# Performance work log

Hardware: AMD Instinct MI355X
Metric: run time of the kernel (lower is better)

Reference implementation:

```python
import jax, jax.numpy as jnp
import numpy as np

N, E, C = 50000, 800000, 192
H1, H2, HF = 256, 512, 512  # grapher mid, grapher conv out, ffn hidden
EPS = 1e-5


def _lin_init(k, out_f, in_f, bias=True):
    s = 1.0 / np.sqrt(in_f)
    kw, kb = jax.random.split(k)
    W = jax.random.uniform(kw, (out_f, in_f), jnp.float32, -s, s)
    if bias:
        b = jax.random.uniform(kb, (out_f,), jnp.float32, -s, s)
        return W, b
    return W


def setup_inputs() -> dict:
    key = jax.random.key(0)
    ks = jax.random.split(key, 10)
    inp = {}
    inp["x"] = jax.random.normal(ks[0], (N, C), jnp.float32)
    inp["edge_index"] = jax.random.randint(ks[1], (2, E), 0, N, jnp.int32)
    # Grapher fc1: Linear(C,256)+BN(256)
    inp["w_g1"], inp["b_g1"] = _lin_init(ks[2], H1, C)
    inp["g1_gamma"], inp["g1_beta"] = jnp.ones((H1,), jnp.float32), jnp.zeros((H1,), jnp.float32)
    # GraphConv(256, 512): lin_rel (with bias) on aggregated neighbors, lin_root (no bias) on self
    inp["w_rel"], inp["b_rel"] = _lin_init(ks[3], H2, H1)
    inp["w_root"] = _lin_init(ks[4], H2, H1, bias=False)
    # Grapher fc2: Linear(512,C)+BN(C)
    inp["w_g2"], inp["b_g2"] = _lin_init(ks[5], C, H2)
    inp["g2_gamma"], inp["g2_beta"] = jnp.ones((C,), jnp.float32), jnp.zeros((C,), jnp.float32)
    # FFN fc1: Linear(C,512)+BN(512)
    inp["w_f1"], inp["b_f1"] = _lin_init(ks[6], HF, C)
    inp["f1_gamma"], inp["f1_beta"] = jnp.ones((HF,), jnp.float32), jnp.zeros((HF,), jnp.float32)
    # FFN fc2: Linear(512,C)+BN(C)
    inp["w_f2"], inp["b_f2"] = _lin_init(ks[7], C, HF)
    inp["f2_gamma"], inp["f2_beta"] = jnp.ones((C,), jnp.float32), jnp.zeros((C,), jnp.float32)
    return inp


def _bn(x, gamma, beta):
    # BatchNorm1d in training mode: biased batch stats over the node dim
    mu = jnp.mean(x, axis=0)
    var = jnp.var(x, axis=0)
    return gamma * (x - mu) * jax.lax.rsqrt(var + EPS) + beta


def reference(x, edge_index, w_g1, b_g1, g1_gamma, g1_beta, w_rel, b_rel, w_root,
              w_g2, b_g2, g2_gamma, g2_beta, w_f1, b_f1, f1_gamma, f1_beta,
              w_f2, b_f2, f2_gamma, f2_beta):
    # ---- Grapher ----
    shortcut = x
    t = _bn(x @ w_g1.T + b_g1, g1_gamma, g1_beta)            # [N, 256]
    src, dst = edge_index[0], edge_index[1]
    agg = jax.ops.segment_sum(t[src], dst, num_segments=t.shape[0])  # [N, 256] 'add' aggregation
    h = agg @ w_rel.T + b_rel + t @ w_root.T                  # [N, 512]
    h = _bn(h @ w_g2.T + b_g2, g2_gamma, g2_beta)             # [N, C]
    x = h + shortcut
    # ---- FFN ----
    shortcut = x
    f = _bn(x @ w_f1.T + b_f1, f1_gamma, f1_beta)             # [N, 512]
    f = jax.nn.gelu(f, approximate=False)
    f = _bn(f @ w_f2.T + b_f2, f2_gamma, f2_beta)             # [N, C]
    return f + shortcut
```

## Files before the change

### kernel.cpp

```cpp
#include <hip/hip_runtime.h>
#include <hip/hip_bf16.h>
#include <math.h>

#define NN 50000
#define EE 800000
#define CC 192

typedef __attribute__((ext_vector_type(4))) float f32x4;
typedef __attribute__((ext_vector_type(8))) short bfx8;
typedef __attribute__((ext_vector_type(8))) unsigned short u16x8;

static __device__ __forceinline__ unsigned short f2bf(float f) {
    return __builtin_bit_cast(unsigned short, __float2bfloat16(f));
}
static __device__ __forceinline__ float b2f(unsigned short u) {
    unsigned v = ((unsigned)u) << 16;
    return __builtin_bit_cast(float, v);
}

template <int MODE>
static __device__ __forceinline__ bfx8 stage_row(const void* Ap, size_t off, int kc,
                                                 const float* __restrict__ Av,
                                                 const float* __restrict__ Bv)
{
    if constexpr (MODE == 1) {
        const float* A = (const float*)Ap;
        float4 u0 = *(const float4*)&A[off], u1 = *(const float4*)&A[off + 4];
        return bfx8{(short)f2bf(u0.x), (short)f2bf(u0.y), (short)f2bf(u0.z), (short)f2bf(u0.w),
                    (short)f2bf(u1.x), (short)f2bf(u1.y), (short)f2bf(u1.z), (short)f2bf(u1.w)};
    } else {
        u16x8 ra = *(const u16x8*)((const unsigned short*)Ap + off);
        if constexpr (MODE == 0) {
            return __builtin_bit_cast(bfx8, ra);
        } else {
            float pa[8], pb[8];
            *(float4*)&pa[0] = *(const float4*)&Av[kc];
            *(float4*)&pa[4] = *(const float4*)&Av[kc + 4];
            *(float4*)&pb[0] = *(const float4*)&Bv[kc];
            *(float4*)&pb[4] = *(const float4*)&Bv[kc + 4];
            bfx8 o;
#pragma unroll
            for (int j = 0; j < 8; ++j) {
                float t = pa[j] * b2f(ra[j]) + pb[j];
                o[j] = (short)f2bf(t);
            }
            return o;
        }
    }
}

#define BM 128
#define BKD 32
#define SA 40
#define CT 136

template <int A1M, int A2M, bool STATS>
__global__ __launch_bounds__(256) void gemm_mfma(
    const void* __restrict__ A1v, const unsigned short* __restrict__ W1,
    const void* __restrict__ A2v, const unsigned short* __restrict__ W2,
    const float* __restrict__ bias,
    const float* __restrict__ Av, const float* __restrict__ Bv,
    unsigned short* __restrict__ outb,
    float* __restrict__ gsum, float* __restrict__ gsq,
    int Nrows, int K, int M)
{
    __shared__ short lds[2][2][BM * SA];
    const int tid  = threadIdx.x;
    const int lane = tid & 63;
    const int wave = tid >> 6;
    const int wm = wave >> 1, wn = wave & 1;

    const int gx = gridDim.x;
    const int nwg = gx * gridDim.y;
    const int linear = blockIdx.y * gx + blockIdx.x;
    const int q = nwg >> 3, r = nwg & 7;
    const int xcd = linear & 7, idx = linear >> 3;
    const int swz = (xcd < r ? xcd * (q + 1) : r * (q + 1) + (xcd - r) * q) + idx;
    const int row0 = (swz / gx) * BM;
    const int col0 = (swz % gx) * BM;

    const int nk = K / BKD;
    const int ntot = (A2M >= 0) ? 2 * nk : nk;

    const int ar = tid >> 2;
    const int ko = (tid & 3) * 8;

    f32x4 acc[4][4];
#pragma unroll
    for (int i = 0; i < 4; ++i)
#pragma unroll
        for (int j = 0; j < 4; ++j) acc[i][j] = f32x4{0.f, 0.f, 0.f, 0.f};

    const int r0c = min(row0 + ar, Nrows - 1);
    const int r1c = min(row0 + ar + 64, Nrows - 1);
    const int c0c = min(col0 + ar, M - 1);
    const int c1c = min(col0 + ar + 64, M - 1);

    auto load_step = [&](int t, bfx8& a0, bfx8& a1, bfx8& b0, bfx8& b1) {
        const int p = (A2M >= 0 && t >= nk) ? 1 : 0;
        const int k0 = (t - p * nk) * BKD;
        const int kc = k0 + ko;
        const unsigned short* W = p ? W2 : W1;
        if (!p) {
            a0 = stage_row<A1M>(A1v, (size_t)r0c * K + kc, kc, Av, Bv);
            a1 = stage_row<A1M>(A1v, (size_t)r1c * K + kc, kc, Av, Bv);
        } else {
            constexpr int M2 = (A2M < 0) ? 0 : A2M;
            a0 = stage_row<M2>(A2v, (size_t)r0c * K + kc, kc, Av, Bv);
            a1 = stage_row<M2>(A2v, (size_t)r1c * K + kc, kc, Av, Bv);
        }
        b0 = *(const bfx8*)&W[(size_t)c0c * K + kc];
        b1 = *(const bfx8*)&W[(size_t)c1c * K + kc];
    };
    auto write_step = [&](int buf, bfx8 a0, bfx8 a1, bfx8 b0, bfx8 b1) {
        *(bfx8*)&lds[buf][0][ar * SA + ko] = a0;
        *(bfx8*)&lds[buf][0][(ar + 64) * SA + ko] = a1;
        *(bfx8*)&lds[buf][1][ar * SA + ko] = b0;
        *(bfx8*)&lds[buf][1][(ar + 64) * SA + ko] = b1;
    };
    auto compute = [&](int buf) {
        const short* Al = lds[buf][0];
        const short* Bl = lds[buf][1];
        bfx8 af[4], bfr[4];
        const int rbase = wm * 64 + (lane & 15);
        const int cbase = wn * 64 + (lane & 15);
        const int kroff = (lane >> 4) * 8;
#pragma unroll
        for (int i = 0; i < 4; ++i) af[i]  = *(const bfx8*)&Al[(rbase + i * 16) * SA + kroff];
#pragma unroll
        for (int j = 0; j < 4; ++j) bfr[j] = *(const bfx8*)&Bl[(cbase + j * 16) * SA + kroff];
#pragma unroll
        for (int i = 0; i < 4; ++i)
#pragma unroll
            for (int j = 0; j < 4; ++j)
                acc[i][j] = __builtin_amdgcn_mfma_f32_16x16x32_bf16(af[i], bfr[j], acc[i][j], 0, 0, 0);
    };

    bfx8 a0, a1, b0, b1;
    load_step(0, a0, a1, b0, b1);
    write_step(0, a0, a1, b0, b1);
    for (int t = 0; t < ntot; ++t) {
        const bool more = (t + 1 < ntot);
        if (more) load_step(t + 1, a0, a1, b0, b1);
        __syncthreads();
        compute(t & 1);
        if (more) write_step((t + 1) & 1, a0, a1, b0, b1);
    }

    __syncthreads();
    short* ctile = &lds[0][0][0];
    float* s_sum = (float*)(&lds[0][0][0] + BM * CT);
    float* s_sq  = s_sum + BM;
    if (STATS && tid < BM) { s_sum[tid] = 0.f; s_sq[tid] = 0.f; }
    float csA[4], cqA[4];
#pragma unroll
    for (int j = 0; j < 4; ++j) {
        const int cl = wn * 64 + j * 16 + (lane & 15);
        const int c = col0 + cl;
        const float bv = (c < M) ? bias[c] : 0.f;
        float cs = 0.f, cq = 0.f;
#pragma unroll
        for (int i = 0; i < 4; ++i) {
            const int rl = wm * 64 + i * 16 + (lane >> 4) * 4;
#pragma unroll
            for (int r2 = 0; r2 < 4; ++r2) {
                const float val = acc[i][j][r2] + bv;
                ctile[(rl + r2) * CT + cl] = (short)f2bf(val);
                if (STATS) {
                    if (row0 + rl + r2 < Nrows) { cs += val; cq += val * val; }
                }
            }
        }
        if (STATS) {
            cs += __shfl_xor(cs, 16); cs += __shfl_xor(cs, 32);
            cq += __shfl_xor(cq, 16); cq += __shfl_xor(cq, 32);
        }
        csA[j] = cs; cqA[j] = cq;
    }
    __syncthreads();
    if (STATS && lane < 16) {
#pragma unroll
        for (int j = 0; j < 4; ++j) {
            const int cl = wn * 64 + j * 16 + lane;
            if (col0 + cl < M) {
                atomicAdd(&s_sum[cl], csA[j]);
                atomicAdd(&s_sq[cl], cqA[j]);
            }
        }
    }
    {
        const int rl0 = tid >> 4;
        const int co  = (tid & 15) * 8;
        const int cg  = col0 + co;
        if (cg < M) {
#pragma unroll
            for (int it = 0; it < 8; ++it) {
                const int rl = rl0 + it * 16;
                const int rg = row0 + rl;
                if (rg < Nrows) {
                    u16x8 v = *(const u16x8*)&ctile[rl * CT + co];
                    *(u16x8*)&outb[(size_t)rg * M + cg] = v;
                }
            }
        }
    }
    if (STATS) {
        __syncthreads();
        if (tid < BM) {
            const int c = col0 + tid;
            if (c < M) {
                atomicAdd(&gsum[c], s_sum[tid]);
                atomicAdd(&gsq[c], s_sq[tid]);
            }
        }
    }
}

#define W_G1 0
#define W_REL 49152
#define W_ROOT 180224
#define W_G2 311296
#define W_F1 409600
#define W_F2 507904
#define W_TOT 606208

__global__ __launch_bounds__(256) void convert_weights(
    const float* __restrict__ w0, const float* __restrict__ w1, const float* __restrict__ w2,
    const float* __restrict__ w3, const float* __restrict__ w4, const float* __restrict__ w5,
    unsigned short* __restrict__ out)
{
    int i = blockIdx.x * 256 + threadIdx.x;
    if (i >= W_TOT) return;
    const float* src; int off;
    if      (i < W_REL)  { src = w0; off = W_G1; }
    else if (i < W_ROOT) { src = w1; off = W_REL; }
    else if (i < W_G2)   { src = w2; off = W_ROOT; }
    else if (i < W_F1)   { src = w3; off = W_G2; }
    else if (i < W_F2)   { src = w4; off = W_F1; }
    else                 { src = w5; off = W_F2; }
    out[i] = f2bf(src[i - off]);
}

__global__ __launch_bounds__(256) void bn_finalize(
    float* __restrict__ sum, float* __restrict__ sumsq,
    const float* __restrict__ g, const float* __restrict__ b,
    float* __restrict__ mu, float* __restrict__ rs,
    float* __restrict__ Av, float* __restrict__ Bv, int M, float invN)
{
    int i = blockIdx.x * 256 + threadIdx.x;
    if (i < 512) {
        if (i < M) {
            float m = sum[i] * invN;
            float v = sumsq[i] * invN - m * m;
            float r = rsqrtf(v + 1e-5f);
            mu[i] = m; rs[i] = r;
            Av[i] = g[i] * r;
            Bv[i] = b[i] - g[i] * m * r;
        }
        sum[i] = 0.f; sumsq[i] = 0.f;
    }
}

template <int MODE>
__global__ __launch_bounds__(256) void bn_apply2(
    const unsigned short* __restrict__ pre, const void* __restrict__ resv,
    void* __restrict__ outv, int total8, int M8,
    const float* __restrict__ g, const float* __restrict__ b,
    const float* __restrict__ mu, const float* __restrict__ rs)
{
    const int i0 = blockIdx.x * 256 + threadIdx.x;
    if (i0 >= total8) return;
    const int c = (i0 % M8) * 8;
    float gg[8], bb[8], mm[8], rr[8];
    *(float4*)&gg[0] = *(const float4*)&g[c];   *(float4*)&gg[4] = *(const float4*)&g[c + 4];
    *(float4*)&bb[0] = *(const float4*)&b[c];   *(float4*)&bb[4] = *(const float4*)&b[c + 4];
    if constexpr (MODE != 1) {
        *(float4*)&mm[0] = *(const float4*)&mu[c];  *(float4*)&mm[4] = *(const float4*)&mu[c + 4];
        *(float4*)&rr[0] = *(const float4*)&rs[c];  *(float4*)&rr[4] = *(const float4*)&rs[c + 4];
    }
    const int stride = gridDim.x * 256;
    for (int i = i0; i < total8; i += stride) {
        u16x8 v = *(const u16x8*)&pre[(size_t)i * 8];
        float t[8];
        if constexpr (MODE == 1) {
#pragma unroll
            for (int k = 0; k < 8; ++k) {
                float u = gg[k] * b2f(v[k]) + bb[k];
                t[k] = 0.5f * u * (1.f + erff(u * 0.70710678118654752f));
            }
            unsigned short* ob = (unsigned short*)outv;
            u16x8 o;
#pragma unroll
            for (int k = 0; k < 8; ++k) o[k] = f2bf(t[k]);
            *(u16x8*)&ob[(size_t)i * 8] = o;
        } else {
#pragma unroll
            for (int k = 0; k < 8; ++k)
                t[k] = gg[k] * (b2f(v[k]) - mm[k]) * rr[k] + bb[k];
            if constexpr (MODE == 2) {
                const float* res = (const float*)resv;
                float4 x0 = *(const float4*)&res[(size_t)i * 8];
                float4 x1 = *(const float4*)&res[(size_t)i * 8 + 4];
                t[0] += x0.x; t[1] += x0.y; t[2] += x0.z; t[3] += x0.w;
                t[4] += x1.x; t[5] += x1.y; t[6] += x1.z; t[7] += x1.w;
                unsigned short* ob = (unsigned short*)outv;
                u16x8 o;
#pragma unroll
                for (int k = 0; k < 8; ++k) o[k] = f2bf(t[k]);
                *(u16x8*)&ob[(size_t)i * 8] = o;
            } else {
                const unsigned short* resb = (const unsigned short*)resv;
                u16x8 xb = *(const u16x8*)&resb[(size_t)i * 8];
#pragma unroll
                for (int k = 0; k < 8; ++k) t[k] += b2f(xb[k]);
                float* outp = (float*)outv;
                *(float4*)&outp[(size_t)i * 8]     = make_float4(t[0], t[1], t[2], t[3]);
                *(float4*)&outp[(size_t)i * 8 + 4] = make_float4(t[4], t[5], t[6], t[7]);
            }
        }
    }
}

__global__ __launch_bounds__(256) void hist_count(
    const int* __restrict__ dst, int* __restrict__ cnt, int E)
{
    int e = blockIdx.x * blockDim.x + threadIdx.x;
    if (e < E) atomicAdd(&cnt[dst[e]], 1);
}

__global__ __launch_bounds__(256) void scan_block_sums(
    const int* __restrict__ cnt, int* __restrict__ partials, int n)
{
    __shared__ int sdata[256];
    int i = blockIdx.x * 256 + threadIdx.x;
    sdata[threadIdx.x] = (i < n) ? cnt[i] : 0;
    __syncthreads();
    for (int s = 128; s > 0; s >>= 1) {
        if (threadIdx.x < s) sdata[threadIdx.x] += sdata[threadIdx.x + s];
        __syncthreads();
    }
    if (threadIdx.x == 0) partials[blockIdx.x] = sdata[0];
}

__global__ __launch_bounds__(256) void scan_partials(
    int* __restrict__ partials, int nb, int* __restrict__ row_start, int n, int E)
{
    __shared__ int sdata[256];
    const int t = threadIdx.x;
    const int v = (t < nb) ? partials[t] : 0;
    sdata[t] = v;
    __syncthreads();
    for (int s = 1; s < 256; s <<= 1) {
        int u = (t >= s) ? sdata[t - s] : 0;
        __syncthreads();
        sdata[t] += u;
        __syncthreads();
    }
    if (t < nb) partials[t] = sdata[t] - v;
    if (t == 0) row_start[n] = E;
}

__global__ __launch_bounds__(256) void scan_final(
    const int* __restrict__ cnt, const int* __restrict__ partials,
    int* __restrict__ row_start, int n)
{
    __shared__ int sdata[256];
    int i = blockIdx.x * 256 + threadIdx.x;
    int v = (i < n) ? cnt[i] : 0;
    sdata[threadIdx.x] = v;
    __syncthreads();
    for (int s = 1; s < 256; s <<= 1) {
        int t = (threadIdx.x >= s) ? sdata[threadIdx.x - s] : 0;
        __syncthreads();
        sdata[threadIdx.x] += t;
        __syncthreads();
    }
    if (i < n) row_start[i] = partials[blockIdx.x] + sdata[threadIdx.x] - v;
}

__global__ __launch_bounds__(256) void csr_fill(
    const int* __restrict__ src, const int* __restrict__ dst,
    const int* __restrict__ row_start, int* __restrict__ cursor,
    int* __restrict__ srcs_sorted, int E)
{
    int e = blockIdx.x * blockDim.x + threadIdx.x;
    if (e < E) {
        int d = dst[e];
        int pos = row_start[d] + atomicAdd(&cursor[d], 1);
        srcs_sorted[pos] = src[e];
    }
}

__global__ __launch_bounds__(256) void gather_sum(
    const int* __restrict__ row_start, const int* __restrict__ srcs,
    const unsigned short* __restrict__ T, unsigned short* __restrict__ AGG,
    const float* __restrict__ Av, const float* __restrict__ Bv, int Nn)
{
    int n = blockIdx.x * 4 + (threadIdx.x >> 6);
    if (n >= Nn) return;
    const int lane = threadIdx.x & 63;
    const int half = lane >> 5;
    const int c0 = (lane & 31) * 8;
    const int e0 = row_start[n], e1 = row_start[n + 1];
    float a[8];
#pragma unroll
    for (int k = 0; k < 8; ++k) a[k] = 0.f;

    int e = e0 + half;
    for (; e + 6 < e1; e += 8) {
        int s0 = srcs[e], s1 = srcs[e + 2], s2 = srcs[e + 4], s3 = srcs[e + 6];
        u16x8 v0 = *(const u16x8*)&T[(size_t)s0 * 256 + c0];
        u16x8 v1 = *(const u16x8*)&T[(size_t)s1 * 256 + c0];
        u16x8 v2 = *(const u16x8*)&T[(size_t)s2 * 256 + c0];
        u16x8 v3 = *(const u16x8*)&T[(size_t)s3 * 256 + c0];
#pragma unroll
        for (int k = 0; k < 8; ++k)
            a[k] += (b2f(v0[k]) + b2f(v1[k])) + (b2f(v2[k]) + b2f(v3[k]));
    }
    for (; e < e1; e += 2) {
        int s = srcs[e];
        u16x8 v = *(const u16x8*)&T[(size_t)s * 256 + c0];
#pragma unroll
        for (int k = 0; k < 8; ++k) a[k] += b2f(v[k]);
    }
#pragma unroll
    for (int k = 0; k < 8; ++k) a[k] += __shfl_xor(a[k], 32);
    if (half == 0) {
        const float deg = (float)(e1 - e0);
        float pa[8], pb[8];
        *(float4*)&pa[0] = *(const float4*)&Av[c0];
        *(float4*)&pa[4] = *(const float4*)&Av[c0 + 4];
        *(float4*)&pb[0] = *(const float4*)&Bv[c0];
        *(float4*)&pb[4] = *(const float4*)&Bv[c0 + 4];
        u16x8 o;
#pragma unroll
        for (int k = 0; k < 8; ++k) o[k] = f2bf(pa[k] * a[k] + deg * pb[k]);
        *(u16x8*)&AGG[(size_t)n * 256 + c0] = o;
    }
}

extern "C" void kernel_launch(void* const* d_in, const int* in_sizes, int n_in,
                              void* d_out, int out_size, void* d_ws, size_t ws_size,
                              hipStream_t stream)
{
    const float* x        = (const float*)d_in[0];
    const int*   ei       = (const int*)d_in[1];
    const float* w_g1     = (const float*)d_in[2];
    const float* b_g1     = (const float*)d_in[3];
    const float* g1_gamma = (const float*)d_in[4];
    const float* g1_beta  = (const float*)d_in[5];
    const float* w_rel    = (const float*)d_in[6];
    const float* b_rel    = (const float*)d_in[7];
    const float* w_root   = (const float*)d_in[8];
    const float* w_g2     = (const float*)d_in[9];
    const float* b_g2     = (const float*)d_in[10];
    const float* g2_gamma = (const float*)d_in[11];
    const float* g2_beta  = (const float*)d_in[12];
    const float* w_f1     = (const float*)d_in[13];
    const float* b_f1     = (const float*)d_in[14];
    const float* f1_gamma = (const float*)d_in[15];
    const float* f1_beta  = (const float*)d_in[16];
    const float* w_f2     = (const float*)d_in[17];
    const float* b_f2     = (const float*)d_in[18];
    const float* f2_gamma = (const float*)d_in[19];
    const float* f2_beta  = (const float*)d_in[20];

    const int* src = ei;
    const int* dst = ei + EE;

    char* p = (char*)d_ws;
    unsigned short* Pre = (unsigned short*)p;   p += (size_t)NN * 512 * 2;
    unsigned short* R2 = (unsigned short*)p;    p += (size_t)NN * 512 * 2;
    unsigned short* R3 = (unsigned short*)p;    p += (size_t)NN * 256 * 2;
    unsigned short* R4 = (unsigned short*)p;    p += (size_t)NN * 256 * 2;
    unsigned short* Wb = (unsigned short*)p;    p += 2 * 1024 * 1024;
    float* sum   = (float*)p;
    float* sumsq = sum + 512;
    float* mu    = sum + 1024;
    float* rs    = sum + 1536;
    float* Avec  = sum + 2048;
    float* Bvec  = sum + 2560;

    unsigned short* AGGb = R4;
    unsigned short* Hb   = R2;
    unsigned short* X2b  = R3;
    unsigned short* Fb   = R2;
    unsigned short* P12  = Pre;

    int* row_start   = (int*)R3;
    int* cnt         = row_start + NN + 16;
    int* cursor      = cnt + NN;
    int* partials    = cursor + NN;
    int* srcs_sorted = partials + 256;

    float* out = (float*)d_out;
    const float invN = 1.f / (float)NN;
    dim3 blk(256);
    const int GY = (NN + 127) / 128;
    const int NB_SCAN = (NN + 255) / 256;
    const int BN_GRID = 1536;

    auto finalize = [&](int M, const float* g, const float* b) {
        hipLaunchKernelGGL(bn_finalize, dim3(2), dim3(256), 0, stream,
                           sum, sumsq, g, b, mu, rs, Avec, Bvec, M, invN);
    };

    hipLaunchKernelGGL(convert_weights, dim3((W_TOT + 255) / 256), blk, 0, stream,
                       w_g1, w_rel, w_root, w_g2, w_f1, w_f2, Wb);
    hipMemsetAsync(sum, 0, 1024 * sizeof(float), stream);

    hipLaunchKernelGGL((gemm_mfma<1, -1, true>), dim3(2, GY), blk, 0, stream,
                       (const void*)x, Wb + W_G1, nullptr, nullptr, b_g1, nullptr, nullptr,
                       Pre, sum, sumsq, NN, CC, 256);
    finalize(256, g1_gamma, g1_beta);
    hipMemsetAsync(cnt, 0, 2 * NN * sizeof(int), stream);
    hipLaunchKernelGGL(hist_count, dim3((EE + 255) / 256), blk, 0, stream, dst, cnt, EE);
    hipLaunchKernelGGL(scan_block_sums, dim3(NB_SCAN), blk, 0, stream, cnt, partials, NN);
    hipLaunchKernelGGL(scan_partials, dim3(1), dim3(256), 0, stream, partials, NB_SCAN,
                       row_start, NN, EE);
    hipLaunchKernelGGL(scan_final, dim3(NB_SCAN), blk, 0, stream, cnt, partials, row_start, NN);
    hipLaunchKernelGGL(csr_fill, dim3((EE + 255) / 256), blk, 0, stream, src, dst,
                       row_start, cursor, srcs_sorted, EE);
    hipLaunchKernelGGL(gather_sum, dim3((NN + 3) / 4), blk, 0, stream,
                       row_start, srcs_sorted, Pre, AGGb, Avec, Bvec, NN);
    hipLaunchKernelGGL((gemm_mfma<0, 2, false>), dim3(4, GY), blk, 0, stream,
                       (const void*)AGGb, Wb + W_REL, (const void*)Pre, Wb + W_ROOT,
                       b_rel, Avec, Bvec, Hb, nullptr, nullptr, NN, 256, 512);
    hipLaunchKernelGGL((gemm_mfma<0, -1, true>), dim3(2, GY), blk, 0, stream,
                       (const void*)Hb, Wb + W_G2, nullptr, nullptr, b_g2, nullptr, nullptr,
                       Pre, sum, sumsq, NN, 512, CC);
    finalize(CC, g2_gamma, g2_beta);
    hipLaunchKernelGGL((bn_apply2<2>), dim3(BN_GRID), blk, 0, stream, Pre, (const void*)x,
                       (void*)X2b, NN * 24, 24, g2_gamma, g2_beta, mu, rs);
    hipLaunchKernelGGL((gemm_mfma<0, -1, true>), dim3(4, GY), blk, 0, stream,
                       (const void*)X2b, Wb + W_F1, nullptr, nullptr, b_f1, nullptr, nullptr,
                       Pre, sum, sumsq, NN, CC, 512);
    finalize(512, f1_gamma, f1_beta);
    hipLaunchKernelGGL((bn_apply2<1>), dim3(BN_GRID), blk, 0, stream, Pre, nullptr,
                       (void*)Fb, NN * 64, 64, Avec, Bvec, nullptr, nullptr);
    hipLaunchKernelGGL((gemm_mfma<0, -1, true>), dim3(2, GY), blk, 0, stream,
                       (const void*)Fb, Wb + W_F2, nullptr, nullptr, b_f2, nullptr, nullptr,
                       P12, sum, sumsq, NN, 512, CC);
    finalize(CC, f2_gamma, f2_beta);
    hipLaunchKernelGGL((bn_apply2<3>), dim3(BN_GRID), blk, 0, stream, P12, (const void*)X2b,
                       (void*)out, NN * 24, 24, f2_gamma, f2_beta, mu, rs);

    (void)in_sizes; (void)n_in; (void)out_size; (void)ws_size;
}
```

Before: 398.9 us.

## Use direct global-to-LDS loads with pre-packed MFMA-fragment weight layout

Weights are pre-packed into a per-tile layout that matches the MFMA fragment order, so each wave can copy B fragments straight from global memory into LDS with global_load_lds. Plain bf16 A operands use the same direct load, and only the converted operands still pass through registers. The goal is to skip the register round-trip and the separate LDS write for staged tiles and to remove padded-stride addressing. The main loop now has a single barrier per step. The cost is six pack launches instead of one, plus the chance of LDS bank conflicts or hazards with the new fragment-linear layout.

```diff
diff --git a/kernel.cpp b/kernel.cpp
--- a/kernel.cpp
+++ b/kernel.cpp
@@ -16,6 +16,14 @@
 static __device__ __forceinline__ float b2f(unsigned short u) {
     unsigned v = ((unsigned)u) << 16;
     return __builtin_bit_cast(float, v);
+}
+
+static __device__ __forceinline__ void gload16(const void* g, void* l) {
+    auto gp = reinterpret_cast<const __attribute__((address_space(1))) unsigned int*>(
+        reinterpret_cast<uintptr_t>(g));
+    auto lp = reinterpret_cast<__attribute__((address_space(3))) unsigned int*>(
+        reinterpret_cast<uintptr_t>(l));
+    __builtin_amdgcn_global_load_lds(gp, lp, 16, 0, 0);
 }
 
 template <int MODE>
@@ -30,41 +38,36 @@
                     (short)f2bf(u1.x), (short)f2bf(u1.y), (short)f2bf(u1.z), (short)f2bf(u1.w)};
     } else {
         u16x8 ra = *(const u16x8*)((const unsigned short*)Ap + off);
-        if constexpr (MODE == 0) {
-            return __builtin_bit_cast(bfx8, ra);
-        } else {
-            float pa[8], pb[8];
-            *(float4*)&pa[0] = *(const float4*)&Av[kc];
-            *(float4*)&pa[4] = *(const float4*)&Av[kc + 4];
-            *(float4*)&pb[0] = *(const float4*)&Bv[kc];
-            *(float4*)&pb[4] = *(const float4*)&Bv[kc + 4];
-            bfx8 o;
-#pragma unroll
-            for (int j = 0; j < 8; ++j) {
-                float t = pa[j] * b2f(ra[j]) + pb[j];
-                o[j] = (short)f2bf(t);
-            }
-            return o;
-        }
+        float pa[8], pb[8];
+        *(float4*)&pa[0] = *(const float4*)&Av[kc];
+        *(float4*)&pa[4] = *(const float4*)&Av[kc + 4];
+        *(float4*)&pb[0] = *(const float4*)&Bv[kc];
+        *(float4*)&pb[4] = *(const float4*)&Bv[kc + 4];
+        bfx8 o;
+#pragma unroll
+        for (int j = 0; j < 8; ++j) {
+            float t = pa[j] * b2f(ra[j]) + pb[j];
+            o[j] = (short)f2bf(t);
+        }
+        return o;
     }
 }
 
 #define BM 128
 #define BKD 32
-#define SA 40
 #define CT 136
 
 template <int A1M, int A2M, bool STATS>
 __global__ __launch_bounds__(256) void gemm_mfma(
-    const void* __restrict__ A1v, const unsigned short* __restrict__ W1,
-    const void* __restrict__ A2v, const unsigned short* __restrict__ W2,
+    const void* __restrict__ A1v, const unsigned short* __restrict__ W1p,
+    const void* __restrict__ A2v, const unsigned short* __restrict__ W2p,
     const float* __restrict__ bias,
     const float* __restrict__ Av, const float* __restrict__ Bv,
     unsigned short* __restrict__ outb,
     float* __restrict__ gsum, float* __restrict__ gsq,
     int Nrows, int K, int M)
 {
-    __shared__ short lds[2][2][BM * SA];
+    __shared__ short smem[17920];
     const int tid  = threadIdx.x;
     const int lane = tid & 63;
     const int wave = tid >> 6;
@@ -78,57 +81,68 @@
     const int swz = (xcd < r ? xcd * (q + 1) : r * (q + 1) + (xcd - r) * q) + idx;
     const int row0 = (swz / gx) * BM;
     const int col0 = (swz % gx) * BM;
+    const int ct = col0 >> 7;
 
     const int nk = K / BKD;
     const int ntot = (A2M >= 0) ? 2 * nk : nk;
 
-    const int ar = tid >> 2;
-    const int ko = (tid & 3) * 8;
-
     f32x4 acc[4][4];
 #pragma unroll
     for (int i = 0; i < 4; ++i)
 #pragma unroll
         for (int j = 0; j < 4; ++j) acc[i][j] = f32x4{0.f, 0.f, 0.f, 0.f};
 
-    const int r0c = min(row0 + ar, Nrows - 1);
-    const int r1c = min(row0 + ar + 64, Nrows - 1);
-    const int c0c = min(col0 + ar, M - 1);
-    const int c1c = min(col0 + ar + 64, M - 1);
-
-    auto load_step = [&](int t, bfx8& a0, bfx8& a1, bfx8& b0, bfx8& b1) {
+    const int f0 = wave * 2, f1 = f0 + 1;
+    const int rowA0 = min(row0 + (f0 >> 2) * 64 + (f0 & 3) * 16 + (lane & 15), Nrows - 1);
+    const int rowA1 = min(row0 + (f1 >> 2) * 64 + (f1 & 3) * 16 + (lane & 15), Nrows - 1);
+
+    auto stage = [&](int t, int buf, bfx8& r0, bfx8& r1) -> bool {
         const int p = (A2M >= 0 && t >= nk) ? 1 : 0;
-        const int k0 = (t - p * nk) * BKD;
-        const int kc = k0 + ko;
-        const unsigned short* W = p ? W2 : W1;
+        const int tt = t - p * nk;
+        const int kc = tt * BKD + (lane >> 4) * 8;
+        short* Ab = &smem[(buf * 2 + 0) * 4096];
+        short* Bb = &smem[(buf * 2 + 1) * 4096];
+        const unsigned short* Wp = p ? W2p : W1p;
+        const size_t tb = (size_t)(ct * nk + tt) * 8;
+        gload16(Wp + (tb + f0) * 512 + lane * 8, Bb + f0 * 512);
+        gload16(Wp + (tb + f1) * 512 + lane * 8, Bb + f1 * 512);
+        bool rm = false;
         if (!p) {
-            a0 = stage_row<A1M>(A1v, (size_t)r0c * K + kc, kc, Av, Bv);
-            a1 = stage_row<A1M>(A1v, (size_t)r1c * K + kc, kc, Av, Bv);
+            if constexpr (A1M == 0) {
+                const unsigned short* A = (const unsigned short*)A1v;
+                gload16(A + (size_t)rowA0 * K + kc, Ab + f0 * 512);
+                gload16(A + (size_t)rowA1 * K + kc, Ab + f1 * 512);
+            } else {
+                r0 = stage_row<A1M>(A1v, (size_t)rowA0 * K + kc, kc, Av, Bv);
+                r1 = stage_row<A1M>(A1v, (size_t)rowA1 * K + kc, kc, Av, Bv);
+                rm = true;
+            }
         } else {
-            constexpr int M2 = (A2M < 0) ? 0 : A2M;
-            a0 = stage_row<M2>(A2v, (size_t)r0c * K + kc, kc, Av, Bv);
-            a1 = stage_row<M2>(A2v, (size_t)r1c * K + kc, kc, Av, Bv);
-        }
-        b0 = *(const bfx8*)&W[(size_t)c0c * K + kc];
-        b1 = *(const bfx8*)&W[(size_t)c1c * K + kc];
+            if constexpr (A2M == 0) {
+                const unsigned short* A = (const unsigned short*)A2v;
+                gload16(A + (size_t)rowA0 * K + kc, Ab + f0 * 512);
+                gload16(A + (size_t)rowA1 * K + kc, Ab + f1 * 512);
+            } else if constexpr (A2M > 0) {
+                r0 = stage_row<A2M>(A2v, (size_t)rowA0 * K + kc, kc, Av, Bv);
+                r1 = stage_row<A2M>(A2v, (size_t)rowA1 * K + kc, kc, Av, Bv);
+                rm = true;
+            }
+        }
+        return rm;
     };
-    auto write_step = [&](int buf, bfx8 a0, bfx8 a1, bfx8 b0, bfx8 b1) {
-        *(bfx8*)&lds[buf][0][ar * SA + ko] = a0;
-        *(bfx8*)&lds[buf][0][(ar + 64) * SA + ko] = a1;
-        *(bfx8*)&lds[buf][1][ar * SA + ko] = b0;
-        *(bfx8*)&lds[buf][1][(ar + 64) * SA + ko] = b1;
+    auto wr = [&](int buf, bfx8 r0, bfx8 r1) {
+        short* Ab = &smem[(buf * 2 + 0) * 4096];
+        *(bfx8*)&Ab[f0 * 512 + lane * 8] = r0;
+        *(bfx8*)&Ab[f1 * 512 + lane * 8] = r1;
     };
     auto compute = [&](int buf) {
-        const short* Al = lds[buf][0];
-        const short* Bl = lds[buf][1];
+        const short* Ab = &smem[(buf * 2 + 0) * 4096];
+        const short* Bb = &smem[(buf * 2 + 1) * 4096];
         bfx8 af[4], bfr[4];
-        const int rbase = wm * 64 + (lane & 15);
-        const int cbase = wn * 64 + (lane & 15);
-        const int kroff = (lane >> 4) * 8;
-#pragma unroll
-        for (int i = 0; i < 4; ++i) af[i]  = *(const bfx8*)&Al[(rbase + i * 16) * SA + kroff];
-#pragma unroll
-        for (int j = 0; j < 4; ++j) bfr[j] = *(const bfx8*)&Bl[(cbase + j * 16) * SA + kroff];
+#pragma unroll
+        for (int i = 0; i < 4; ++i) af[i]  = *(const bfx8*)&Ab[(wm * 4 + i) * 512 + lane * 8];
+#pragma unroll
+        for (int j = 0; j < 4; ++j) bfr[j] = *(const bfx8*)&Bb[(wn * 4 + j) * 512 + lane * 8];
 #pragma unroll
         for (int i = 0; i < 4; ++i)
 #pragma unroll
@@ -136,20 +150,24 @@
                 acc[i][j] = __builtin_amdgcn_mfma_f32_16x16x32_bf16(af[i], bfr[j], acc[i][j], 0, 0, 0);
     };
 
-    bfx8 a0, a1, b0, b1;
-    load_step(0, a0, a1, b0, b1);
-    write_step(0, a0, a1, b0, b1);
+    {
+        bfx8 r0, r1;
+        bool rm = stage(0, 0, r0, r1);
+        if (rm) wr(0, r0, r1);
+    }
+    __syncthreads();
     for (int t = 0; t < ntot; ++t) {
-        const bool more = (t + 1 < ntot);
-        if (more) load_step(t + 1, a0, a1, b0, b1);
-        __syncthreads();
-        compute(t & 1);
-        if (more) write_step((t + 1) & 1, a0, a1, b0, b1);
-    }
-
-    __syncthreads();
-    short* ctile = &lds[0][0][0];
-    float* s_sum = (float*)(&lds[0][0][0] + BM * CT);
+        const int buf = t & 1;
+        bfx8 n0, n1;
+        bool rmn = false;
+        if (t + 1 < ntot) rmn = stage(t + 1, buf ^ 1, n0, n1);
+        compute(buf);
+        if (rmn) wr(buf ^ 1, n0, n1);
+        __syncthreads();
+    }
+
+    short* ctile = smem;
+    float* s_sum = (float*)&smem[BM * CT];
     float* s_sq  = s_sum + BM;
     if (STATS && tid < BM) { s_sum[tid] = 0.f; s_sq[tid] = 0.f; }
     float csA[4], cqA[4];
@@ -216,29 +234,26 @@
     }
 }
 
-#define W_G1 0
-#define W_REL 49152
-#define W_ROOT 180224
-#define W_G2 311296
-#define W_F1 409600
-#define W_F2 507904
-#define W_TOT 606208
-
-__global__ __launch_bounds__(256) void convert_weights(
-    const float* __restrict__ w0, const float* __restrict__ w1, const float* __restrict__ w2,
-    const float* __restrict__ w3, const float* __restrict__ w4, const float* __restrict__ w5,
-    unsigned short* __restrict__ out)
-{
-    int i = blockIdx.x * 256 + threadIdx.x;
-    if (i >= W_TOT) return;
-    const float* src; int off;
-    if      (i < W_REL)  { src = w0; off = W_G1; }
-    else if (i < W_ROOT) { src = w1; off = W_REL; }
-    else if (i < W_G2)   { src = w2; off = W_ROOT; }
-    else if (i < W_F1)   { src = w3; off = W_G2; }
-    else if (i < W_F2)   { src = w4; off = W_F1; }
-    else                 { src = w5; off = W_F2; }
-    out[i] = f2bf(src[i - off]);
+__global__ __launch_bounds__(256) void pack_weight(
+    const float* __restrict__ W, unsigned short* __restrict__ dst,
+    int M, int K, int total)
+{
+    int tid = blockIdx.x * 256 + threadIdx.x;
+    if (tid >= total) return;
+    int lane = tid & 63;
+    int f = (tid >> 6) & 7;
+    int tile = tid >> 9;
+    int nk = K >> 5;
+    int t = tile % nk, ct = tile / nk;
+    int col = ct * 128 + (f >> 2) * 64 + (f & 3) * 16 + (lane & 15);
+    col = min(col, M - 1);
+    int k0 = t * 32 + (lane >> 4) * 8;
+    const float* s = &W[(size_t)col * K + k0];
+    float4 u0 = *(const float4*)s, u1 = *(const float4*)(s + 4);
+    ushort4 d0 = {f2bf(u0.x), f2bf(u0.y), f2bf(u0.z), f2bf(u0.w)};
+    ushort4 d1 = {f2bf(u1.x), f2bf(u1.y), f2bf(u1.z), f2bf(u1.w)};
+    *(ushort4*)&dst[(size_t)tid * 8] = d0;
+    *(ushort4*)&dst[(size_t)tid * 8 + 4] = d1;
 }
 
 __global__ __launch_bounds__(256) void bn_finalize(
@@ -438,6 +453,13 @@
         *(u16x8*)&AGG[(size_t)n * 256 + c0] = o;
     }
 }
+
+#define P_G1   0
+#define P_REL  49152
+#define P_ROOT 180224
+#define P_G2   311296
+#define P_F1   442368
+#define P_F2   540672
 
 extern "C" void kernel_launch(void* const* d_in, const int* in_sizes, int n_in,
                               void* d_out, int out_size, void* d_ws, size_t ws_size,
@@ -504,13 +526,22 @@
         hipLaunchKernelGGL(bn_finalize, dim3(2), dim3(256), 0, stream,
                            sum, sumsq, g, b, mu, rs, Avec, Bvec, M, invN);
     };
-
-    hipLaunchKernelGGL(convert_weights, dim3((W_TOT + 255) / 256), blk, 0, stream,
-                       w_g1, w_rel, w_root, w_g2, w_f1, w_f2, Wb);
+    auto pack = [&](const float* W, unsigned short* dstp, int M, int K, int Mpad) {
+        int total = Mpad * K / 8;
+        hipLaunchKernelGGL(pack_weight, dim3((total + 255) / 256), blk, 0, stream,
+                           W, dstp, M, K, total);
+    };
+
+    pack(w_g1,   Wb + P_G1,   256, 192, 256);
+    pack(w_rel,  Wb + P_REL,  512, 256, 512);
+    pack(w_root, Wb + P_ROOT, 512, 256, 512);
+    pack(w_g2,   Wb + P_G2,   192, 512, 256);
+    pack(w_f1,   Wb + P_F1,   512, 192, 512);
+    pack(w_f2,   Wb + P_F2,   192, 512, 256);
     hipMemsetAsync(sum, 0, 1024 * sizeof(float), stream);
 
     hipLaunchKernelGGL((gemm_mfma<1, -1, true>), dim3(2, GY), blk, 0, stream,
-                       (const void*)x, Wb + W_G1, nullptr, nullptr, b_g1, nullptr, nullptr,
+                       (const void*)x, Wb + P_G1, nullptr, nullptr, b_g1, nullptr, nullptr,
                        Pre, sum, sumsq, NN, CC, 256);
     finalize(256, g1_gamma, g1_beta);
     hipMemsetAsync(cnt, 0, 2 * NN * sizeof(int), stream);
@@ -524,22 +555,22 @@
     hipLaunchKernelGGL(gather_sum, dim3((NN + 3) / 4), blk, 0, stream,
                        row_start, srcs_sorted, Pre, AGGb, Avec, Bvec, NN);
     hipLaunchKernelGGL((gemm_mfma<0, 2, false>), dim3(4, GY), blk, 0, stream,
-                       (const void*)AGGb, Wb + W_REL, (const void*)Pre, Wb + W_ROOT,
+                       (const void*)AGGb, Wb + P_REL, (const void*)Pre, Wb + P_ROOT,
                        b_rel, Avec, Bvec, Hb, nullptr, nullptr, NN, 256, 512);
     hipLaunchKernelGGL((gemm_mfma<0, -1, true>), dim3(2, GY), blk, 0, stream,
-                       (const void*)Hb, Wb + W_G2, nullptr, nullptr, b_g2, nullptr, nullptr,
+                       (const void*)Hb, Wb + P_G2, nullptr, nullptr, b_g2, nullptr, nullptr,
                        Pre, sum, sumsq, NN, 512, CC);
     finalize(CC, g2_gamma, g2_beta);
     hipLaunchKernelGGL((bn_apply2<2>), dim3(BN_GRID), blk, 0, stream, Pre, (const void*)x,
                        (void*)X2b, NN * 24, 24, g2_gamma, g2_beta, mu, rs);
     hipLaunchKernelGGL((gemm_mfma<0, -1, true>), dim3(4, GY), blk, 0, stream,
-                       (const void*)X2b, Wb + W_F1, nullptr, nullptr, b_f1, nullptr, nullptr,
+                       (const void*)X2b, Wb + P_F1, nullptr, nullptr, b_f1, nullptr, nullptr,
                        Pre, sum, sumsq, NN, CC, 512);
     finalize(512, f1_gamma, f1_beta);
     hipLaunchKernelGGL((bn_apply2<1>), dim3(BN_GRID), blk, 0, stream, Pre, nullptr,
                        (void*)Fb, NN * 64, 64, Avec, Bvec, nullptr, nullptr);
     hipLaunchKernelGGL((gemm_mfma<0, -1, true>), dim3(2, GY), blk, 0, stream,
-                       (const void*)Fb, Wb + W_F2, nullptr, nullptr, b_f2, nullptr, nullptr,
+                       (const void*)Fb, Wb + P_F2, nullptr, nullptr, b_f2, nullptr, nullptr,
                        P12, sum, sumsq, NN, 512, CC);
     finalize(CC, f2_gamma, f2_beta);
     hipLaunchKernelGGL((bn_apply2<3>), dim3(BN_GRID), blk, 0, stream, P12, (const void*)X2b,
```

Measured after the change: 442.4 us. +10.9%, slower.
